# Optimization experiments

Measured on AMD Instinct MI355X. Metric: run time of the kernel, lower is better.

## Reference

```python
import jax, jax.numpy as jnp
import numpy as np

SIZE = 512
N_STROKES = 8
N_SAMPLES = 32
STROKE_WIDTH = 0.04


def setup_inputs() -> dict:
    key = jax.random.key(0)
    k1, _ = jax.random.split(key)
    # control points seeded like torch.rand(...) * 0.6 + 0.2
    control_points = jax.random.uniform(k1, (N_STROKES, 4, 2), dtype=jnp.float32) * 0.6 + 0.2
    # pixel grid buffer: (x, y) coords in [0,1], row-major over (y, x)
    coords = jnp.linspace(0.0, 1.0, SIZE, dtype=jnp.float32)
    grid_y, grid_x = jnp.meshgrid(coords, coords, indexing="ij")
    pixel_grid = jnp.stack([grid_x, grid_y], axis=-1).reshape(-1, 2)  # (HW, 2)
    return {"control_points": control_points, "pixel_grid": pixel_grid}


def _bezier3_samples(curves, n_samples):
    # curves: (S, 4, 2) -> (S, n_samples, 2)
    ts = jnp.linspace(0.0, 1.0, n_samples, dtype=curves.dtype)
    t = ts[None, :, None]
    mt = 1.0 - t
    p0, p1, p2, p3 = (curves[:, k:k + 1, :] for k in range(4))
    return mt ** 3 * p0 + 3.0 * mt ** 2 * t * p1 + 3.0 * mt * t ** 2 * p2 + t ** 3 * p3


def reference(control_points, pixel_grid):
    # all_strokes(): symmetric=False, empty stroke_groups -> just clamp
    pts = jnp.clip(control_points, 0.0, 1.0)
    samples = _bezier3_samples(pts, N_SAMPLES).reshape(-1, 2)  # (P, 2), P = S*n_samples
    sharpness = float(N_SAMPLES) * 8.0
    # pairwise distances (HW, P) — soft-min via logsumexp over curve points
    diff = pixel_grid[:, None, :] - samples[None, :, :]          # (HW, P, 2)
    dist = jnp.sqrt(jnp.sum(diff * diff, axis=-1))               # (HW, P)
    min_dist = -jax.nn.logsumexp(-sharpness * dist, axis=-1) / sharpness  # (HW,)
    coverage = jax.nn.sigmoid((STROKE_WIDTH - min_dist) * (8.0 / STROKE_WIDTH))
    return (1.0 - coverage.reshape(SIZE, SIZE))[None]  # (1, H, W)
```

## Files before the change

kernel.cpp:

```cpp
#include <hip/hip_runtime.h>


#define SIZE 512
#define RADIUS 0.06f
#define FARCUT 0.1217f
#define HB 0.00684932f
#define HD 0.00968631f

__device__ __forceinline__ float clamp01(float x) {
    return fminf(fmaxf(x, 0.0f), 1.0f);
}
__device__ __forceinline__ float wave_min(float v) {
    #pragma unroll
    for (int m = 1; m < 64; m <<= 1) v = fminf(v, __shfl_xor(v, m));
    return v;
}

__global__ __launch_bounds__(64) void bezier_glyph_kernel(
        const float* __restrict__ cp,
        float* __restrict__ out)
{
    __shared__ float2 list[260];

    const int tid = threadIdx.x;
    const int b   = blockIdx.x;
    const int row_base = (b >> 6) << 3;
    const int col_base = (b & 63) << 3;
    const float inv = 1.0f / 511.0f;
    const float cx  = ((float)col_base + 3.5f) * inv;
    const float cy  = ((float)row_base + 3.5f) * inv;

    float sxv[4], syv[4], bb2v[4];
    {
        const int s = tid >> 3;
        const float* p = cp + s * 8;
        const float x0 = clamp01(p[0]), y0 = clamp01(p[1]);
        const float x1 = clamp01(p[2]), y1 = clamp01(p[3]);
        const float x2 = clamp01(p[4]), y2 = clamp01(p[5]);
        const float x3 = clamp01(p[6]), y3 = clamp01(p[7]);
        const float c1x = 3.0f * (x1 - x0);
        const float c2x = 3.0f * (x0 - 2.0f * x1 + x2);
        const float c3x = x3 - x0 + 3.0f * (x1 - x2);
        const float c1y = 3.0f * (y1 - y0);
        const float c2y = 3.0f * (y0 - 2.0f * y1 + y2);
        const float c3y = y3 - y0 + 3.0f * (y1 - y2);
        #pragma unroll
        for (int r = 0; r < 4; ++r) {
            const int j    = ((tid << 2) + r) & 31;
            const float u  = (float)j * (1.0f / 31.0f);
            const float sx = fmaf(fmaf(fmaf(c3x, u, c2x), u, c1x), u, x0);
            const float sy = fmaf(fmaf(fmaf(c3y, u, c2y), u, c1y), u, y0);
            sxv[r] = sx; syv[r] = sy;
            const float bx = fmaxf(fabsf(sx - cx) - HB, 0.0f);
            const float by = fmaxf(fabsf(sy - cy) - HB, 0.0f);
            bb2v[r] = fmaf(bx, bx, by * by);
        }
    }

    const float A = __builtin_amdgcn_sqrtf(wave_min(
        fminf(fminf(bb2v[0], bb2v[1]), fminf(bb2v[2], bb2v[3]))));

    const int row = row_base + (tid >> 3);
    const int col = col_base + (tid & 7);

    if (A > FARCUT) {
        out[row * SIZE + col] = 1.0f;
        return;
    }

    const float T   = fminf(A + 2.0f * HD, FARCUT) + RADIUS + 1e-4f;
    const float Ts  = T * T;
    const unsigned long long lt = (1ull << tid) - 1ull;
    int n = 0;
    #pragma unroll
    for (int r = 0; r < 4; ++r) {
        const bool keep = (bb2v[r] <= Ts);
        const unsigned long long mk = __ballot(keep);
        if (keep)
            list[n + (int)__popcll(mk & lt)] = make_float2(sxv[r], syv[r]);
        n += (int)__popcll(mk);
    }
    if (tid < 4) list[n + tid] = make_float2(1e3f, 1e3f);
    __syncthreads();

    const float py = (float)row * inv;
    const float px = (float)col * inv;
    const float C  = 369.3299304675766f;
    const float nC = -C;
    const float cA = C * A;
    float S = 0.0f;
    const int nr = (n + 3) & ~3;
    for (int k = 0; k < nr; k += 4) {
        const float2 a = list[k],     b2 = list[k + 1];
        const float2 c = list[k + 2], e  = list[k + 3];
        float dx, dy;
        dx = px - a.x;  dy = py - a.y;  const float qa = fmaf(dx, dx, dy * dy);
        dx = px - b2.x; dy = py - b2.y; const float qb = fmaf(dx, dx, dy * dy);
        dx = px - c.x;  dy = py - c.y;  const float qc = fmaf(dx, dx, dy * dy);
        dx = px - e.x;  dy = py - e.y;  const float qe = fmaf(dx, dx, dy * dy);
        S += __builtin_amdgcn_exp2f(fmaf(nC, __builtin_amdgcn_sqrtf(qa), cA))
           + __builtin_amdgcn_exp2f(fmaf(nC, __builtin_amdgcn_sqrtf(qb), cA))
           + __builtin_amdgcn_exp2f(fmaf(nC, __builtin_amdgcn_sqrtf(qc), cA))
           + __builtin_amdgcn_exp2f(fmaf(nC, __builtin_amdgcn_sqrtf(qe), cA));
    }

    const float md = A - __builtin_amdgcn_logf(S) * (1.0f / C);
    const float K  = 288.53900817779268f;
    out[row * SIZE + col] = __builtin_amdgcn_rcpf(
        1.0f + __builtin_amdgcn_exp2f((0.04f - md) * K));
}

extern "C" void kernel_launch(void* const* d_in, const int* in_sizes, int n_in,
                              void* d_out, int out_size, void* d_ws, size_t ws_size,
                              hipStream_t stream) {
    const float* cp = (const float*)d_in[0];
    float* out = (float*)d_out;
    bezier_glyph_kernel<<<dim3(4096), dim3(64), 0, stream>>>(cp, out);
}
```

Baseline: 58.49 us.

## Split each tile's candidate-point loop across two waves with shared-memory reduction

Each 8x8 pixel tile now uses two wavefronts instead of one. The 256 curve samples are interleaved between the waves, each wave builds its own candidate list and computes partial exp sums, and wave 0 combines the two partial sums from shared memory and writes the output. The intent is to halve the serial per-pixel loop length and raise parallelism, at the cost of extra barriers, a block-level min reduction, and a second wave that only does redundant setup for far tiles.

```diff
diff --git a/kernel.cpp b/kernel.cpp
--- a/kernel.cpp
+++ b/kernel.cpp
@@ -16,24 +16,30 @@
     return v;
 }
 
-__global__ __launch_bounds__(64) void bezier_glyph_kernel(
+__global__ __launch_bounds__(128, 8) void bezier_glyph_kernel(
         const float* __restrict__ cp,
         float* __restrict__ out)
 {
-    __shared__ float2 list[260];
+    __shared__ float2 lists[2][136];
+    __shared__ float  aMin[2];
+    __shared__ float  redS[128];
 
-    const int tid = threadIdx.x;
-    const int b   = blockIdx.x;
+    const int tid  = threadIdx.x;
+    const int lane = tid & 63;
+    const int wid  = tid >> 6;
+
+    const int b        = blockIdx.x;
     const int row_base = (b >> 6) << 3;
     const int col_base = (b & 63) << 3;
     const float inv = 1.0f / 511.0f;
     const float cx  = ((float)col_base + 3.5f) * inv;
     const float cy  = ((float)row_base + 3.5f) * inv;
 
-    float sxv[4], syv[4], bb2v[4];
-    {
-        const int s = tid >> 3;
-        const float* p = cp + s * 8;
+    float sxv[2], syv[2], bb2v[2];
+    #pragma unroll
+    for (int r = 0; r < 2; ++r) {
+        const int k = (r << 7) + (lane << 1) + wid;
+        const float* p = cp + ((k >> 5) << 3);
         const float x0 = clamp01(p[0]), y0 = clamp01(p[1]);
         const float x1 = clamp01(p[2]), y1 = clamp01(p[3]);
         const float x2 = clamp01(p[4]), y2 = clamp01(p[5]);
@@ -44,43 +50,44 @@
         const float c1y = 3.0f * (y1 - y0);
         const float c2y = 3.0f * (y0 - 2.0f * y1 + y2);
         const float c3y = y3 - y0 + 3.0f * (y1 - y2);
-        #pragma unroll
-        for (int r = 0; r < 4; ++r) {
-            const int j    = ((tid << 2) + r) & 31;
-            const float u  = (float)j * (1.0f / 31.0f);
-            const float sx = fmaf(fmaf(fmaf(c3x, u, c2x), u, c1x), u, x0);
-            const float sy = fmaf(fmaf(fmaf(c3y, u, c2y), u, c1y), u, y0);
-            sxv[r] = sx; syv[r] = sy;
-            const float bx = fmaxf(fabsf(sx - cx) - HB, 0.0f);
-            const float by = fmaxf(fabsf(sy - cy) - HB, 0.0f);
-            bb2v[r] = fmaf(bx, bx, by * by);
-        }
+        const float u  = (float)(k & 31) * (1.0f / 31.0f);
+        const float sx = fmaf(fmaf(fmaf(c3x, u, c2x), u, c1x), u, x0);
+        const float sy = fmaf(fmaf(fmaf(c3y, u, c2y), u, c1y), u, y0);
+        sxv[r] = sx; syv[r] = sy;
+        const float bx = fmaxf(fabsf(sx - cx) - HB, 0.0f);
+        const float by = fmaxf(fabsf(sy - cy) - HB, 0.0f);
+        bb2v[r] = fmaf(bx, bx, by * by);
     }
 
-    const float A = __builtin_amdgcn_sqrtf(wave_min(
-        fminf(fminf(bb2v[0], bb2v[1]), fminf(bb2v[2], bb2v[3]))));
+    {
+        const float wm = wave_min(fminf(bb2v[0], bb2v[1]));
+        if (lane == 0) aMin[wid] = wm;
+    }
+    __syncthreads();
+    const float A = __builtin_amdgcn_sqrtf(fminf(aMin[0], aMin[1]));
 
-    const int row = row_base + (tid >> 3);
-    const int col = col_base + (tid & 7);
+    const int row = row_base + (lane >> 3);
+    const int col = col_base + (lane & 7);
 
     if (A > FARCUT) {
-        out[row * SIZE + col] = 1.0f;
+        if (wid == 0) out[row * SIZE + col] = 1.0f;
         return;
     }
 
-    const float T   = fminf(A + 2.0f * HD, FARCUT) + RADIUS + 1e-4f;
-    const float Ts  = T * T;
-    const unsigned long long lt = (1ull << tid) - 1ull;
+    const float T  = fminf(A + 2.0f * HD, FARCUT) + RADIUS + 1e-4f;
+    const float Ts = T * T;
+    const unsigned long long lt = (1ull << lane) - 1ull;
+    float2* mylist = lists[wid];
     int n = 0;
     #pragma unroll
-    for (int r = 0; r < 4; ++r) {
+    for (int r = 0; r < 2; ++r) {
         const bool keep = (bb2v[r] <= Ts);
         const unsigned long long mk = __ballot(keep);
         if (keep)
-            list[n + (int)__popcll(mk & lt)] = make_float2(sxv[r], syv[r]);
+            mylist[n + (int)__popcll(mk & lt)] = make_float2(sxv[r], syv[r]);
         n += (int)__popcll(mk);
     }
-    if (tid < 4) list[n + tid] = make_float2(1e3f, 1e3f);
+    if (lane < 4) mylist[n + lane] = make_float2(1e3f, 1e3f);
     __syncthreads();
 
     const float py = (float)row * inv;
@@ -91,8 +98,8 @@
     float S = 0.0f;
     const int nr = (n + 3) & ~3;
     for (int k = 0; k < nr; k += 4) {
-        const float2 a = list[k],     b2 = list[k + 1];
-        const float2 c = list[k + 2], e  = list[k + 3];
+        const float2 a = mylist[k],     b2 = mylist[k + 1];
+        const float2 c = mylist[k + 2], e  = mylist[k + 3];
         float dx, dy;
         dx = px - a.x;  dy = py - a.y;  const float qa = fmaf(dx, dx, dy * dy);
         dx = px - b2.x; dy = py - b2.y; const float qb = fmaf(dx, dx, dy * dy);
@@ -103,11 +110,16 @@
            + __builtin_amdgcn_exp2f(fmaf(nC, __builtin_amdgcn_sqrtf(qc), cA))
            + __builtin_amdgcn_exp2f(fmaf(nC, __builtin_amdgcn_sqrtf(qe), cA));
     }
+    redS[tid] = S;
+    __syncthreads();
 
-    const float md = A - __builtin_amdgcn_logf(S) * (1.0f / C);
-    const float K  = 288.53900817779268f;
-    out[row * SIZE + col] = __builtin_amdgcn_rcpf(
-        1.0f + __builtin_amdgcn_exp2f((0.04f - md) * K));
+    if (wid == 0) {
+        const float St = redS[lane] + redS[64 + lane];
+        const float md = A - __builtin_amdgcn_logf(St) * (1.0f / C);
+        const float K  = 288.53900817779268f;
+        out[row * SIZE + col] = __builtin_amdgcn_rcpf(
+            1.0f + __builtin_amdgcn_exp2f((0.04f - md) * K));
+    }
 }
 
 extern "C" void kernel_launch(void* const* d_in, const int* in_sizes, int n_in,
@@ -115,5 +127,5 @@
                               hipStream_t stream) {
     const float* cp = (const float*)d_in[0];
     float* out = (float*)d_out;
-    bezier_glyph_kernel<<<dim3(4096), dim3(64), 0, stream>>>(cp, out);
+    bezier_glyph_kernel<<<dim3(4096), dim3(128), 0, stream>>>(cp, out);
 }
```

After: 59.01 us. No clear change (+0.9%).
